# Kernel tuning notes

Hardware: AMD Instinct MI355X
Metric: run time of the kernel (lower is better)

## Reference

```python
import jax, jax.numpy as jnp
import numpy as np

NUM_LEVELS = 4
RADIUS = 4


def _avg_pool2(x):
    # x: [N, H, W] -> [N, H//2, W//2], 2x2 mean pool, stride 2 (F.avg_pool2d(corr,2,2))
    N, H, W = x.shape
    return x.reshape(N, H // 2, 2, W // 2, 2).mean(axis=(2, 4))


def _bilinear_sample(img, x, y):
    # img: [N, H, W]; x, y: [N, P] pixel coords.
    # Matches F.grid_sample(..., mode='bilinear', align_corners=True, padding_mode='zeros')
    # after the pixel->normalized->pixel round trip in bilinear_sampler (identity).
    N, H, W = img.shape
    x0 = jnp.floor(x)
    y0 = jnp.floor(y)
    wx = x - x0
    wy = y - y0
    x0i = x0.astype(jnp.int32)
    y0i = y0.astype(jnp.int32)
    flat = img.reshape(N, H * W)

    def gather(yi, xi):
        valid = (xi >= 0) & (xi <= W - 1) & (yi >= 0) & (yi <= H - 1)
        idx = jnp.clip(yi, 0, H - 1) * W + jnp.clip(xi, 0, W - 1)
        v = jnp.take_along_axis(flat, idx, axis=1)
        return jnp.where(valid, v, jnp.zeros((), img.dtype))

    v00 = gather(y0i, x0i)
    v01 = gather(y0i, x0i + 1)
    v10 = gather(y0i + 1, x0i)
    v11 = gather(y0i + 1, x0i + 1)
    return (v00 * (1 - wy) * (1 - wx) + v01 * (1 - wy) * wx
            + v10 * wy * (1 - wx) + v11 * wy * wx)


def _corr_block(fmap1, fmap2, coords):
    B, D, H, W = fmap1.shape
    # all-pairs correlation: [B, H*W, H*W] / sqrt(D)
    f1 = fmap1.reshape(B, D, H * W)
    f2 = fmap2.reshape(B, D, H * W)
    corr = jnp.einsum('bdn,bdm->bnm', f1, f2) / jnp.sqrt(jnp.asarray(D, fmap1.dtype))
    corr = corr.reshape(B * H * W, H, W)
    pyramid = [corr]
    for _ in range(NUM_LEVELS - 1):
        corr = _avg_pool2(corr)
        pyramid.append(corr)

    # coords: [B, 2, H, W] (x, y) -> [B*H*W, 2]
    c = coords.transpose(0, 2, 3, 1).reshape(B * H * W, 2)
    r = RADIUS
    d = jnp.linspace(-r, r, 2 * r + 1)
    dyg, dxg = jnp.meshgrid(d, d, indexing='ij')
    # faithful to torch: delta = stack(meshgrid(dy, dx), -1); channel 0 added to x, 1 to y
    delta = jnp.stack([dyg, dxg], axis=-1).reshape(-1, 2)  # [81, 2]

    outs = []
    for i, lvl in enumerate(pyramid):
        cl = c[:, None, :] / (2.0 ** i) + delta[None, :, :]  # [N, 81, 2]
        s = _bilinear_sample(lvl, cl[..., 0], cl[..., 1])    # [N, 81]
        outs.append(s.reshape(B, H, W, (2 * r + 1) ** 2))
    out = jnp.concatenate(outs, axis=-1)                     # [B, H, W, 4*81]
    return out.transpose(0, 3, 1, 2).astype(jnp.float32)


def setup_inputs() -> dict:
    key = jax.random.key(0)
    k1, k2, k3 = jax.random.split(key, 3)
    B, D, H, W = 2, 256, 80, 80
    fmap1 = jax.random.normal(k1, (B, D, H, W), dtype=jnp.float32)
    fmap2 = jax.random.normal(k2, (B, D, H, W), dtype=jnp.float32)
    # pixel coords in [0, W-1] x [0, H-1] (channel 0 = x, channel 1 = y)
    u = jax.random.uniform(k3, (B, 2, H, W), dtype=jnp.float32)
    scale = jnp.asarray([W - 1, H - 1], jnp.float32).reshape(1, 2, 1, 1)
    coords = u * scale
    return {"fmap1": fmap1, "fmap2": fmap2, "coords": coords}


def reference(fmap1, fmap2, coords):
    return _corr_block(fmap1, fmap2, coords)
```

## Files before the change

kernel.cpp:

```cpp
#include <hip/hip_runtime.h>


typedef _Float16 h2 __attribute__((ext_vector_type(2)));
typedef _Float16 half8 __attribute__((ext_vector_type(8)));
typedef float f32x4 __attribute__((ext_vector_type(4)));

#define HWDIM 80
#define DCH 256
#define NPIX 12800
#define NBUCKET 800
#define CHP 352

__global__ __launch_bounds__(256) void zero_k(float4* __restrict__ dst) {
    int i = blockIdx.x * 256 + threadIdx.x;
    dst[i] = make_float4(0.f, 0.f, 0.f, 0.f);
}

__global__ __launch_bounds__(256) void transpose_all(const float* __restrict__ f1,
                                                     const float* __restrict__ f2,
                                                     _Float16* __restrict__ f1h,
                                                     _Float16* __restrict__ f2p0) {
    __shared__ float tile[256][33];
    int bid = blockIdx.x;
    bool isf1 = bid < 400;
    int lb = isf1 ? bid : bid - 400;
    const float* src = isf1 ? f1 : f2;
    int b = lb / 200;
    int s0 = (lb % 200) * 32;
    int t = threadIdx.x;
    const float* sb = src + (size_t)b * DCH * (HWDIM * HWDIM);
#pragma unroll 4
    for (int k = 0; k < 32; ++k) {
        int j = t + 256 * k;
        int c = j >> 5, s = j & 31;
        tile[c][s] = sb[(size_t)c * (HWDIM * HWDIM) + s0 + s];
    }
    __syncthreads();
    int p = t & 127;
    int srow = t >> 7;
    if (isf1) {
        _Float16* db = f1h + ((size_t)b * 6400 + s0) * DCH;
#pragma unroll 4
        for (int k = 0; k < 16; ++k) {
            int s = 2 * k + srow;
            h2 v;
            v[0] = (_Float16)tile[2 * p][s];
            v[1] = (_Float16)tile[2 * p + 1][s];
            *(h2*)(db + (size_t)s * DCH + 2 * p) = v;
        }
    } else {
#pragma unroll 4
        for (int k = 0; k < 16; ++k) {
            int s = 2 * k + srow;
            int spatial = s0 + s;
            int yy = spatial / 80;
            int xx = spatial - yy * 80;
            h2 v;
            v[0] = (_Float16)tile[2 * p][s];
            v[1] = (_Float16)tile[2 * p + 1][s];
            size_t off = (size_t)b * 2073600 + (size_t)(p >> 4) * 259200
                       + ((size_t)(yy + 5) * 90 + (xx + 5)) * 32 + ((2 * p) & 31);
            *(h2*)(f2p0 + off) = v;
        }
    }
}

__global__ __launch_bounds__(256) void pools(const _Float16* __restrict__ l0,
                                             _Float16* __restrict__ l1,
                                             _Float16* __restrict__ l2,
                                             _Float16* __restrict__ l3) {
    int i = blockIdx.x * 256 + threadIdx.x;
    if (i < 409600) {
        int c2 = i & 15;
        int r = i >> 4;
        int x = r % 40; r /= 40;
        int y = r % 40; r /= 40;
        int pl = r & 7;
        int b = r >> 3;
        const h2* s = (const h2*)l0 + (size_t)b * 1036800 + (size_t)pl * 129600
                    + ((size_t)(2 * y + 5) * 90 + (2 * x + 5)) * 16 + c2;
        h2 v00 = s[0], v01 = s[16], v10 = s[90 * 16], v11 = s[90 * 16 + 16];
        float r0 = ((float)v00[0] + (float)v01[0] + (float)v10[0] + (float)v11[0]) * 0.25f;
        float r1 = ((float)v00[1] + (float)v01[1] + (float)v10[1] + (float)v11[1]) * 0.25f;
        h2 o; o[0] = (_Float16)r0; o[1] = (_Float16)r1;
        *((h2*)l1 + (size_t)b * 320000 + (size_t)pl * 40000
          + ((size_t)(y + 5) * 50 + (x + 5)) * 16 + c2) = o;
    } else if (i < 512000) {
        int j = i - 409600;
        int c2 = j & 15;
        int r = j >> 4;
        int x = r % 20; r /= 20;
        int y = r % 20; r /= 20;
        int pl = r & 7;
        int b = r >> 3;
        const h2* s = (const h2*)l0 + (size_t)b * 1036800 + (size_t)pl * 129600 + c2;
        float r0 = 0.f, r1 = 0.f;
#pragma unroll
        for (int dy = 0; dy < 4; ++dy)
#pragma unroll
            for (int dx = 0; dx < 4; ++dx) {
                h2 v = s[((size_t)(4 * y + dy + 5) * 90 + (4 * x + dx + 5)) * 16];
                r0 += (float)v[0];
                r1 += (float)v[1];
            }
        h2 o; o[0] = (_Float16)(r0 * 0.0625f); o[1] = (_Float16)(r1 * 0.0625f);
        *((h2*)l2 + (size_t)b * 115200 + (size_t)pl * 14400
          + ((size_t)(y + 5) * 30 + (x + 5)) * 16 + c2) = o;
    } else {
        int j = i - 512000;
        int c2 = j & 15;
        int r = j >> 4;
        int x = r % 10; r /= 10;
        int y = r % 10; r /= 10;
        int pl = r & 7;
        int b = r >> 3;
        const h2* s = (const h2*)l0 + (size_t)b * 1036800 + (size_t)pl * 129600 + c2;
        float r0 = 0.f, r1 = 0.f;
#pragma unroll
        for (int dy = 0; dy < 8; ++dy)
#pragma unroll
            for (int dx = 0; dx < 8; ++dx) {
                h2 v = s[((size_t)(8 * y + dy + 5) * 90 + (8 * x + dx + 5)) * 16];
                r0 += (float)v[0];
                r1 += (float)v[1];
            }
        h2 o; o[0] = (_Float16)(r0 * 0.015625f); o[1] = (_Float16)(r1 * 0.015625f);
        *((h2*)l3 + (size_t)b * 51200 + (size_t)pl * 6400
          + ((size_t)(y + 5) * 20 + (x + 5)) * 16 + c2) = o;
    }
}

static __device__ __forceinline__ int bucket_of(const float* coords, int n) {
    int b = n / 6400;
    int r = n - b * 6400;
    float cx = coords[(size_t)b * 12800 + r];
    float cy = coords[(size_t)b * 12800 + 6400 + r];
    int ix = min(max((int)floorf(cx), 0), 79);
    int iy = min(max((int)floorf(cy), 0), 79);
    return b * 400 + (iy >> 2) * 20 + (ix >> 2);
}

__global__ __launch_bounds__(1024) void bucket_k(const float* __restrict__ coords,
                                                 int* __restrict__ sortedIdxP,
                                                 int* __restrict__ rank) {
    __shared__ unsigned int histS[NBUCKET], startS[NBUCKET], curS[NBUCKET];
    __shared__ unsigned int waveSum[16];
    __shared__ unsigned int totalS;
    int t = threadIdx.x;
    if (t < NBUCKET) histS[t] = 0u;
    __syncthreads();
    int bkt[13];
#pragma unroll
    for (int i = 0; i < 13; ++i) {
        int n = i * 1024 + t;
        if (n < NPIX) {
            bkt[i] = bucket_of(coords, n);
            atomicAdd(&histS[bkt[i]], 1u);
        }
    }
    __syncthreads();
    unsigned int v = (t < NBUCKET) ? ((histS[t] + 15u) & ~15u) : 0u;
    unsigned int x = v;
#pragma unroll
    for (int d = 1; d < 64; d <<= 1) {
        unsigned int y = __shfl_up(x, d);
        if ((t & 63) >= d) x += y;
    }
    if ((t & 63) == 63) waveSum[t >> 6] = x;
    __syncthreads();
    if (t < 16) {
        unsigned int w = waveSum[t];
#pragma unroll
        for (int d = 1; d < 16; d <<= 1) {
            unsigned int y = __shfl_up(w, d);
            if (t >= d) w += y;
        }
        waveSum[t] = w;
    }
    __syncthreads();
    unsigned int incl = x + ((t >> 6) ? waveSum[(t >> 6) - 1] : 0u);
    if (t < NBUCKET) {
        unsigned int e = incl - v;
        startS[t] = e;
        curS[t] = e;
        if (t == NBUCKET - 1) totalS = incl;
    }
    __syncthreads();
#pragma unroll
    for (int i = 0; i < 13; ++i) {
        int n = i * 1024 + t;
        if (n < NPIX) {
            unsigned int pos = atomicAdd(&curS[bkt[i]], 1u);
            sortedIdxP[pos] = n;
            rank[n] = (int)pos;
        }
    }
    __syncthreads();
    if (t < NBUCKET) {
        unsigned int h = histS[t];
        if (h) {
            unsigned int pc = (h + 15u) & ~15u;
            unsigned int base = startS[t];
            int dup = sortedIdxP[base];
            for (unsigned int s = h; s < pc; ++s) sortedIdxP[base + s] = dup;
        }
    }
    for (unsigned int s = totalS + t; s < 25600u; s += 1024u) sortedIdxP[s] = -1;
}

template <int TB, int TE>
static __device__ __forceinline__ void run_tiles(
    int lane, int b,
    const _Float16* __restrict__ f2p0, const _Float16* __restrict__ f2p1,
    const _Float16* __restrict__ f2p2, const _Float16* __restrict__ f2p3,
    const int* X0cS, const int* Y0cS, const half8* bf, _Float16* G) {
#pragma unroll
    for (int tt = TB; tt < TE; ++tt) {
        const int L  = tt < 11 ? 0 : tt < 19 ? 1 : tt < 26 ? 2 : 3;
        const int rt = tt - (L == 0 ? 0 : L == 1 ? 11 : L == 2 ? 19 : 26);
        const int Ww = L == 0 ? 13 : L == 1 ? 11 : 10;
        const int MT = L == 0 ? 169 : L == 1 ? 121 : 100;
        const int MAG = L == 0 ? 161320 : L == 1 ? 190652 : 209716;
        const int Wp = L == 0 ? 90 : L == 1 ? 50 : L == 2 ? 30 : 20;
        const int PS = L == 0 ? 259200 : L == 1 ? 80000 : L == 2 ? 28800 : 12800;
        const int PB = L == 0 ? 2073600 : L == 1 ? 640000 : L == 2 ? 230400 : 102400;
        const int GO = L == 0 ? 0 : L == 1 ? 176 : L == 2 ? 304 : 416;
        const _Float16* f2L = (L == 0 ? f2p0 : L == 1 ? f2p1 : L == 2 ? f2p2 : f2p3);
        const _Float16* f2b = f2L + (size_t)b * PB
                            + ((size_t)(Y0cS[L] + 5) * Wp + (X0cS[L] + 5)) * 32;
        int m = min(rt * 16 + (lane & 15), MT - 1);
        int my = (m * MAG) >> 21;
        int mx = m - my * Ww;
        const float4* ap = (const float4*)(f2b + (size_t)(my * Wp + mx) * 32)
                         + (lane >> 4);
        half8 av[8];
#pragma unroll
        for (int kk = 0; kk < 8; ++kk)
            av[kk] = __builtin_bit_cast(half8, ap[kk * (PS / 8)]);
        __builtin_amdgcn_sched_barrier(0);
        f32x4 acc0 = {0.f, 0.f, 0.f, 0.f};
        f32x4 acc1 = {0.f, 0.f, 0.f, 0.f};
#pragma unroll
        for (int kk = 0; kk < 8; kk += 2) {
            acc0 = __builtin_amdgcn_mfma_f32_16x16x32_f16(av[kk], bf[kk], acc0, 0, 0, 0);
            acc1 = __builtin_amdgcn_mfma_f32_16x16x32_f16(av[kk + 1], bf[kk + 1], acc1, 0, 0, 0);
        }
        int gr = GO + rt * 16 + (lane >> 4) * 4;
#pragma unroll
        for (int r = 0; r < 4; ++r)
            G[(gr + r) * 17 + (lane & 15)] = (_Float16)(acc0[r] + acc1[r]);
    }
}

__global__ __launch_bounds__(512, 4) void corr_mfma(
    const _Float16* __restrict__ f1h,
    const _Float16* __restrict__ f2p0, const _Float16* __restrict__ f2p1,
    const _Float16* __restrict__ f2p2, const _Float16* __restrict__ f2p3,
    const float* __restrict__ coords, const int* __restrict__ sortedIdxP,
    _Float16* __restrict__ scratch) {
    __shared__ _Float16 G[528 * 17];
    __shared__ _Float16 f1S[16 * 264];
    __shared__ float fxS[4][16], fyS[4][16];
    __shared__ int lxS[4][16], lyS[4][16];
    __shared__ int X0cS[4], Y0cS[4], bS;

    int pphys = blockIdx.x;
    int l = (pphys & 7) * 200 + (pphys >> 3);
    int tid = threadIdx.x;
    if (sortedIdxP[l * 16] < 0) return;
    int lane = tid & 63;
    int wave = tid >> 6;

    {
        int px = tid >> 5, q = tid & 31;
        int n = sortedIdxP[l * 16 + px];
        const float4* src = (const float4*)(f1h + (size_t)n * DCH);
        *((float4*)(f1S + px * 264) + q) = src[q];
    }
    if (tid < 64) {
        int px = tid & 15, Lt = tid >> 4;
        int n = sortedIdxP[l * 16 + px];
        int b = n / 6400;
        int r = n - b * 6400;
        float cx = coords[(size_t)b * 12800 + r];
        float cy = coords[(size_t)b * 12800 + 6400 + r];
        float ls = 1.0f / (float)(1 << Lt);
        float cxl = cx * ls, cyl = cy * ls;
        float fxf = floorf(cxl), fyf = floorf(cyl);
        int X0 = (int)fxf - 4, Y0 = (int)fyf - 4;
        int ix = min(max((int)floorf(cx), 0), 79);
        int iy = min(max((int)floorf(cy), 0), 79);
        int X0c = (((ix >> 2) * 4) >> Lt) - 4;
        int Y0c = (((iy >> 2) * 4) >> Lt) - 4;
        lxS[Lt][px] = min(max(X0 - X0c, 0), 3);
        lyS[Lt][px] = min(max(Y0 - Y0c, 0), 3);
        fxS[Lt][px] = cxl - fxf;
        fyS[Lt][px] = cyl - fyf;
        X0cS[Lt] = X0c;
        Y0cS[Lt] = Y0c;
        if (tid == 0) bS = sortedIdxP[l * 16] / 6400;
    }
    __syncthreads();
    int b = bS;

    half8 bf[8];
#pragma unroll
    for (int kk = 0; kk < 8; ++kk)
        bf[kk] = *(const half8*)(f1S + (lane & 15) * 264 + ((lane >> 4) + 4 * kk) * 8);

    if      (wave == 0) run_tiles<0, 5>(lane, b, f2p0, f2p1, f2p2, f2p3, X0cS, Y0cS, bf, G);
    else if (wave == 1) run_tiles<5, 9>(lane, b, f2p0, f2p1, f2p2, f2p3, X0cS, Y0cS, bf, G);
    else if (wave == 2) run_tiles<9, 13>(lane, b, f2p0, f2p1, f2p2, f2p3, X0cS, Y0cS, bf, G);
    else if (wave == 3) run_tiles<13, 17>(lane, b, f2p0, f2p1, f2p2, f2p3, X0cS, Y0cS, bf, G);
    else if (wave == 4) run_tiles<17, 21>(lane, b, f2p0, f2p1, f2p2, f2p3, X0cS, Y0cS, bf, G);
    else if (wave == 5) run_tiles<21, 25>(lane, b, f2p0, f2p1, f2p2, f2p3, X0cS, Y0cS, bf, G);
    else if (wave == 6) run_tiles<25, 29>(lane, b, f2p0, f2p1, f2p2, f2p3, X0cS, Y0cS, bf, G);
    else                run_tiles<29, 33>(lane, b, f2p0, f2p1, f2p2, f2p3, X0cS, Y0cS, bf, G);
    __syncthreads();

    _Float16* sc = scratch + (size_t)l * 16 * CHP;
    for (int idx = tid; idx < 5184; idx += 512) {
        int k2 = idx >> 4, x = idx & 15;
        int Le = (k2 * 810) >> 16;
        int k = k2 - Le * 81;
        int Ww = Le == 0 ? 13 : Le == 1 ? 11 : 10;
        int GO = Le == 0 ? 0 : Le == 1 ? 176 : Le == 2 ? 304 : 416;
        int a = (k * 57) >> 9;
        int c = k - 9 * a;
        int gx = lxS[Le][x] + a, gy = lyS[Le][x] + c;
        int m00 = GO + gy * Ww + gx;
        float fx = fxS[Le][x], fy = fyS[Le][x];
        float t00 = (float)G[m00 * 17 + x];
        float t01 = (float)G[(m00 + 1) * 17 + x];
        float t10 = (float)G[(m00 + Ww) * 17 + x];
        float t11 = (float)G[(m00 + Ww + 1) * 17 + x];
        float v = ((1.f - fy) * ((1.f - fx) * t00 + fx * t01)
                 + fy * ((1.f - fx) * t10 + fx * t11)) * 0.0625f;
        sc[x * CHP + k2] = (_Float16)v;
    }
}

__global__ __launch_bounds__(256) void unsort_t(const _Float16* __restrict__ scratch,
                                                const int* __restrict__ rank,
                                                float* __restrict__ out) {
    __shared__ _Float16 lds[64][40];
    int blk = blockIdx.x;
    int b = blk / 100;
    int nl0 = (blk % 100) * 64;
    int t = threadIdx.x;
    int p = t >> 2, j = t & 3;
    int n = blk * 64 + p;
    int rk = rank[n];
    const float4* src = (const float4*)(scratch + (size_t)rk * CHP);
    int px = t & 63, iq = t >> 6;

    for (int c = 0; c < 11; ++c) {
        float4 f4 = src[c * 4 + j];
        *(float4*)(&lds[p][j * 8]) = f4;
        __syncthreads();
#pragma unroll
        for (int w = 0; w < 8; ++w) {
            int i = w * 4 + iq;
            int ch = c * 32 + i;
            if (ch < 324)
                out[((size_t)b * 324 + ch) * 6400 + nl0 + px] = (float)lds[px][i];
        }
        __syncthreads();
    }
}

extern "C" void kernel_launch(void* const* d_in, const int* in_sizes, int n_in,
                              void* d_out, int out_size, void* d_ws, size_t ws_size,
                              hipStream_t stream) {
    const float* fmap1 = (const float*)d_in[0];
    const float* fmap2 = (const float*)d_in[1];
    const float* coords = (const float*)d_in[2];
    float* out = (float*)d_out;
    char* ws = (char*)d_ws;

    _Float16* f1h  = (_Float16*)(ws);
    _Float16* f2p0 = (_Float16*)(ws + 6553600);
    _Float16* f2p1 = (_Float16*)(ws + 14848000);
    _Float16* f2p2 = (_Float16*)(ws + 17408000);
    _Float16* f2p3 = (_Float16*)(ws + 18329600);
    int* sortedIdxP = (int*)(ws + 18739200);
    int* rank       = (int*)(ws + 18841600);
    _Float16* scratch = (_Float16*)(ws + 18892800);

    zero_k<<<dim3(2975), dim3(256), 0, stream>>>((float4*)f2p0);

    transpose_all<<<dim3(800), dim3(256), 0, stream>>>(fmap1, fmap2, f1h, f2p0);
    pools<<<dim3(2100), dim3(256), 0, stream>>>(f2p0, f2p1, f2p2, f2p3);
    bucket_k<<<dim3(1), dim3(1024), 0, stream>>>(coords, sortedIdxP, rank);
    corr_mfma<<<dim3(1600), dim3(512), 0, stream>>>(f1h, f2p0, f2p1, f2p2, f2p3,
                                                    coords, sortedIdxP, scratch);
    unsort_t<<<dim3(200), dim3(256), 0, stream>>>(scratch, rank, out);
}
```

Measured before the change: 98.22 us.

## Software-pipeline f2 tile loads across MFMA tiles and coalesce scratch writes

After: 91.06 us. 1.08x faster.

```diff
diff --git a/kernel.cpp b/kernel.cpp
--- a/kernel.cpp
+++ b/kernel.cpp
@@ -208,51 +208,85 @@
     for (unsigned int s = totalS + t; s < 25600u; s += 1024u) sortedIdxP[s] = -1;
 }
 
+template <int TT> struct TC {
+    static constexpr int L   = TT < 11 ? 0 : TT < 19 ? 1 : TT < 26 ? 2 : 3;
+    static constexpr int rt  = TT - (L == 0 ? 0 : L == 1 ? 11 : L == 2 ? 19 : 26);
+    static constexpr int Ww  = L == 0 ? 13 : L == 1 ? 11 : 10;
+    static constexpr int MT_ = L == 0 ? 169 : L == 1 ? 121 : 100;
+    static constexpr int MAG = L == 0 ? 161320 : L == 1 ? 190652 : 209716;
+    static constexpr int Wp  = L == 0 ? 90 : L == 1 ? 50 : L == 2 ? 30 : 20;
+    static constexpr int PS  = L == 0 ? 259200 : L == 1 ? 80000 : L == 2 ? 28800 : 12800;
+    static constexpr int PB  = L == 0 ? 2073600 : L == 1 ? 640000 : L == 2 ? 230400 : 102400;
+    static constexpr int GO  = L == 0 ? 0 : L == 1 ? 176 : L == 2 ? 304 : 416;
+};
+
+template <int TT>
+static __device__ __forceinline__ void tile_load(
+    int lane, int b,
+    const _Float16* __restrict__ f2p0, const _Float16* __restrict__ f2p1,
+    const _Float16* __restrict__ f2p2, const _Float16* __restrict__ f2p3,
+    const int* X0cS, const int* Y0cS, half8 (&av)[8]) {
+    using C = TC<TT>;
+    const _Float16* f2L = (C::L == 0 ? f2p0 : C::L == 1 ? f2p1 : C::L == 2 ? f2p2 : f2p3);
+    const _Float16* f2b = f2L + (size_t)b * C::PB
+                        + ((size_t)(Y0cS[C::L] + 5) * C::Wp + (X0cS[C::L] + 5)) * 32;
+    int m = min(C::rt * 16 + (lane & 15), C::MT_ - 1);
+    int my = (m * C::MAG) >> 21;
+    int mx = m - my * C::Ww;
+    const float4* ap = (const float4*)(f2b + (size_t)(my * C::Wp + mx) * 32) + (lane >> 4);
+#pragma unroll
+    for (int kk = 0; kk < 8; ++kk)
+        av[kk] = __builtin_bit_cast(half8, ap[kk * (C::PS / 8)]);
+}
+
+template <int TT>
+static __device__ __forceinline__ void tile_mfma(
+    int lane, const half8 (&av)[8], const half8* bf, _Float16* G) {
+    using C = TC<TT>;
+    f32x4 acc0 = {0.f, 0.f, 0.f, 0.f};
+    f32x4 acc1 = {0.f, 0.f, 0.f, 0.f};
+#pragma unroll
+    for (int kk = 0; kk < 8; kk += 2) {
+        acc0 = __builtin_amdgcn_mfma_f32_16x16x32_f16(av[kk], bf[kk], acc0, 0, 0, 0);
+        acc1 = __builtin_amdgcn_mfma_f32_16x16x32_f16(av[kk + 1], bf[kk + 1], acc1, 0, 0, 0);
+    }
+    int gr = C::GO + C::rt * 16 + (lane >> 4) * 4;
+#pragma unroll
+    for (int r = 0; r < 4; ++r)
+        G[(gr + r) * 17 + (lane & 15)] = (_Float16)(acc0[r] + acc1[r]);
+}
+
+template <int TT, int TE>
+static __device__ __forceinline__ void run_pipe(
+    int lane, int b,
+    const _Float16* __restrict__ f2p0, const _Float16* __restrict__ f2p1,
+    const _Float16* __restrict__ f2p2, const _Float16* __restrict__ f2p3,
+    const int* X0cS, const int* Y0cS, const half8* bf, _Float16* G,
+    half8 (&avCur)[8]) {
+    if constexpr (TT + 1 < TE) {
+        half8 avNext[8];
+        tile_load<TT + 1>(lane, b, f2p0, f2p1, f2p2, f2p3, X0cS, Y0cS, avNext);
+        __builtin_amdgcn_sched_barrier(0);
+        tile_mfma<TT>(lane, avCur, bf, G);
+        run_pipe<TT + 1, TE>(lane, b, f2p0, f2p1, f2p2, f2p3, X0cS, Y0cS, bf, G, avNext);
+    } else {
+        __builtin_amdgcn_sched_barrier(0);
+        tile_mfma<TT>(lane, avCur, bf, G);
+    }
+}
+
 template <int TB, int TE>
 static __device__ __forceinline__ void run_tiles(
     int lane, int b,
     const _Float16* __restrict__ f2p0, const _Float16* __restrict__ f2p1,
     const _Float16* __restrict__ f2p2, const _Float16* __restrict__ f2p3,
     const int* X0cS, const int* Y0cS, const half8* bf, _Float16* G) {
-#pragma unroll
-    for (int tt = TB; tt < TE; ++tt) {
-        const int L  = tt < 11 ? 0 : tt < 19 ? 1 : tt < 26 ? 2 : 3;
-        const int rt = tt - (L == 0 ? 0 : L == 1 ? 11 : L == 2 ? 19 : 26);
-        const int Ww = L == 0 ? 13 : L == 1 ? 11 : 10;
-        const int MT = L == 0 ? 169 : L == 1 ? 121 : 100;
-        const int MAG = L == 0 ? 161320 : L == 1 ? 190652 : 209716;
-        const int Wp = L == 0 ? 90 : L == 1 ? 50 : L == 2 ? 30 : 20;
-        const int PS = L == 0 ? 259200 : L == 1 ? 80000 : L == 2 ? 28800 : 12800;
-        const int PB = L == 0 ? 2073600 : L == 1 ? 640000 : L == 2 ? 230400 : 102400;
-        const int GO = L == 0 ? 0 : L == 1 ? 176 : L == 2 ? 304 : 416;
-        const _Float16* f2L = (L == 0 ? f2p0 : L == 1 ? f2p1 : L == 2 ? f2p2 : f2p3);
-        const _Float16* f2b = f2L + (size_t)b * PB
-                            + ((size_t)(Y0cS[L] + 5) * Wp + (X0cS[L] + 5)) * 32;
-        int m = min(rt * 16 + (lane & 15), MT - 1);
-        int my = (m * MAG) >> 21;
-        int mx = m - my * Ww;
-        const float4* ap = (const float4*)(f2b + (size_t)(my * Wp + mx) * 32)
-                         + (lane >> 4);
-        half8 av[8];
-#pragma unroll
-        for (int kk = 0; kk < 8; ++kk)
-            av[kk] = __builtin_bit_cast(half8, ap[kk * (PS / 8)]);
-        __builtin_amdgcn_sched_barrier(0);
-        f32x4 acc0 = {0.f, 0.f, 0.f, 0.f};
-        f32x4 acc1 = {0.f, 0.f, 0.f, 0.f};
-#pragma unroll
-        for (int kk = 0; kk < 8; kk += 2) {
-            acc0 = __builtin_amdgcn_mfma_f32_16x16x32_f16(av[kk], bf[kk], acc0, 0, 0, 0);
-            acc1 = __builtin_amdgcn_mfma_f32_16x16x32_f16(av[kk + 1], bf[kk + 1], acc1, 0, 0, 0);
-        }
-        int gr = GO + rt * 16 + (lane >> 4) * 4;
-#pragma unroll
-        for (int r = 0; r < 4; ++r)
-            G[(gr + r) * 17 + (lane & 15)] = (_Float16)(acc0[r] + acc1[r]);
-    }
-}
-
-__global__ __launch_bounds__(512, 4) void corr_mfma(
+    half8 av0[8];
+    tile_load<TB>(lane, b, f2p0, f2p1, f2p2, f2p3, X0cS, Y0cS, av0);
+    run_pipe<TB, TE>(lane, b, f2p0, f2p1, f2p2, f2p3, X0cS, Y0cS, bf, G, av0);
+}
+
+__global__ __launch_bounds__(512, 2) void corr_mfma(
     const _Float16* __restrict__ f1h,
     const _Float16* __restrict__ f2p0, const _Float16* __restrict__ f2p1,
     const _Float16* __restrict__ f2p2, const _Float16* __restrict__ f2p3,
@@ -319,8 +353,10 @@
     __syncthreads();
 
     _Float16* sc = scratch + (size_t)l * 16 * CHP;
-    for (int idx = tid; idx < 5184; idx += 512) {
-        int k2 = idx >> 4, x = idx & 15;
+    for (int idx = tid; idx < 16 * CHP; idx += 512) {
+        int x = idx / CHP;
+        int k2 = idx - x * CHP;
+        if (k2 >= 324) continue;
         int Le = (k2 * 810) >> 16;
         int k = k2 - Le * 81;
         int Ww = Le == 0 ? 13 : Le == 1 ? 11 : 10;
@@ -336,7 +372,7 @@
         float t11 = (float)G[(m00 + Ww + 1) * 17 + x];
         float v = ((1.f - fy) * ((1.f - fx) * t00 + fx * t01)
                  + fy * ((1.f - fx) * t10 + fx * t11)) * 0.0625f;
-        sc[x * CHP + k2] = (_Float16)v;
+        sc[idx] = (_Float16)v;
     }
 }
 
```

## Split corr_mfma work per pixel group across two blocks by pyramid level

Applied to the files above, without the earlier changes.

Measured after the change: 94.61 us. 1.04x faster.

```diff
diff --git a/kernel.cpp b/kernel.cpp
--- a/kernel.cpp
+++ b/kernel.cpp
@@ -210,7 +210,7 @@
 
 template <int TB, int TE>
 static __device__ __forceinline__ void run_tiles(
-    int lane, int b,
+    int lane, int b, int goff,
     const _Float16* __restrict__ f2p0, const _Float16* __restrict__ f2p1,
     const _Float16* __restrict__ f2p2, const _Float16* __restrict__ f2p3,
     const int* X0cS, const int* Y0cS, const half8* bf, _Float16* G) {
@@ -245,7 +245,7 @@
             acc0 = __builtin_amdgcn_mfma_f32_16x16x32_f16(av[kk], bf[kk], acc0, 0, 0, 0);
             acc1 = __builtin_amdgcn_mfma_f32_16x16x32_f16(av[kk + 1], bf[kk + 1], acc1, 0, 0, 0);
         }
-        int gr = GO + rt * 16 + (lane >> 4) * 4;
+        int gr = GO - goff + rt * 16 + (lane >> 4) * 4;
 #pragma unroll
         for (int r = 0; r < 4; ++r)
             G[(gr + r) * 17 + (lane & 15)] = (_Float16)(acc0[r] + acc1[r]);
@@ -258,14 +258,16 @@
     const _Float16* __restrict__ f2p2, const _Float16* __restrict__ f2p3,
     const float* __restrict__ coords, const int* __restrict__ sortedIdxP,
     _Float16* __restrict__ scratch) {
-    __shared__ _Float16 G[528 * 17];
+    __shared__ _Float16 G[352 * 17];
     __shared__ _Float16 f1S[16 * 264];
     __shared__ float fxS[4][16], fyS[4][16];
     __shared__ int lxS[4][16], lyS[4][16];
     __shared__ int X0cS[4], Y0cS[4], bS;
 
     int pphys = blockIdx.x;
-    int l = (pphys & 7) * 200 + (pphys >> 3);
+    int lh = (pphys & 7) * 400 + (pphys >> 3);
+    int l = lh >> 1;
+    int h = lh & 1;
     int tid = threadIdx.x;
     if (sortedIdxP[l * 16] < 0) return;
     int lane = tid & 63;
@@ -308,35 +310,67 @@
     for (int kk = 0; kk < 8; ++kk)
         bf[kk] = *(const half8*)(f1S + (lane & 15) * 264 + ((lane >> 4) + 4 * kk) * 8);
 
-    if      (wave == 0) run_tiles<0, 5>(lane, b, f2p0, f2p1, f2p2, f2p3, X0cS, Y0cS, bf, G);
-    else if (wave == 1) run_tiles<5, 9>(lane, b, f2p0, f2p1, f2p2, f2p3, X0cS, Y0cS, bf, G);
-    else if (wave == 2) run_tiles<9, 13>(lane, b, f2p0, f2p1, f2p2, f2p3, X0cS, Y0cS, bf, G);
-    else if (wave == 3) run_tiles<13, 17>(lane, b, f2p0, f2p1, f2p2, f2p3, X0cS, Y0cS, bf, G);
-    else if (wave == 4) run_tiles<17, 21>(lane, b, f2p0, f2p1, f2p2, f2p3, X0cS, Y0cS, bf, G);
-    else if (wave == 5) run_tiles<21, 25>(lane, b, f2p0, f2p1, f2p2, f2p3, X0cS, Y0cS, bf, G);
-    else if (wave == 6) run_tiles<25, 29>(lane, b, f2p0, f2p1, f2p2, f2p3, X0cS, Y0cS, bf, G);
-    else                run_tiles<29, 33>(lane, b, f2p0, f2p1, f2p2, f2p3, X0cS, Y0cS, bf, G);
+    if (h == 0) {
+        if      (wave == 0) run_tiles<0, 2>(lane, b, 0, f2p0, f2p1, f2p2, f2p3, X0cS, Y0cS, bf, G);
+        else if (wave == 1) run_tiles<2, 4>(lane, b, 0, f2p0, f2p1, f2p2, f2p3, X0cS, Y0cS, bf, G);
+        else if (wave == 2) run_tiles<4, 6>(lane, b, 0, f2p0, f2p1, f2p2, f2p3, X0cS, Y0cS, bf, G);
+        else if (wave == 3) run_tiles<6, 7>(lane, b, 0, f2p0, f2p1, f2p2, f2p3, X0cS, Y0cS, bf, G);
+        else if (wave == 4) run_tiles<7, 8>(lane, b, 0, f2p0, f2p1, f2p2, f2p3, X0cS, Y0cS, bf, G);
+        else if (wave == 5) run_tiles<8, 9>(lane, b, 0, f2p0, f2p1, f2p2, f2p3, X0cS, Y0cS, bf, G);
+        else if (wave == 6) run_tiles<9, 10>(lane, b, 0, f2p0, f2p1, f2p2, f2p3, X0cS, Y0cS, bf, G);
+        else                run_tiles<10, 11>(lane, b, 0, f2p0, f2p1, f2p2, f2p3, X0cS, Y0cS, bf, G);
+    } else {
+        if      (wave == 0) run_tiles<11, 14>(lane, b, 176, f2p0, f2p1, f2p2, f2p3, X0cS, Y0cS, bf, G);
+        else if (wave == 1) run_tiles<14, 17>(lane, b, 176, f2p0, f2p1, f2p2, f2p3, X0cS, Y0cS, bf, G);
+        else if (wave == 2) run_tiles<17, 20>(lane, b, 176, f2p0, f2p1, f2p2, f2p3, X0cS, Y0cS, bf, G);
+        else if (wave == 3) run_tiles<20, 23>(lane, b, 176, f2p0, f2p1, f2p2, f2p3, X0cS, Y0cS, bf, G);
+        else if (wave == 4) run_tiles<23, 26>(lane, b, 176, f2p0, f2p1, f2p2, f2p3, X0cS, Y0cS, bf, G);
+        else if (wave == 5) run_tiles<26, 29>(lane, b, 176, f2p0, f2p1, f2p2, f2p3, X0cS, Y0cS, bf, G);
+        else if (wave == 6) run_tiles<29, 31>(lane, b, 176, f2p0, f2p1, f2p2, f2p3, X0cS, Y0cS, bf, G);
+        else                run_tiles<31, 33>(lane, b, 176, f2p0, f2p1, f2p2, f2p3, X0cS, Y0cS, bf, G);
+    }
     __syncthreads();
 
     _Float16* sc = scratch + (size_t)l * 16 * CHP;
-    for (int idx = tid; idx < 5184; idx += 512) {
-        int k2 = idx >> 4, x = idx & 15;
-        int Le = (k2 * 810) >> 16;
-        int k = k2 - Le * 81;
-        int Ww = Le == 0 ? 13 : Le == 1 ? 11 : 10;
-        int GO = Le == 0 ? 0 : Le == 1 ? 176 : Le == 2 ? 304 : 416;
-        int a = (k * 57) >> 9;
-        int c = k - 9 * a;
-        int gx = lxS[Le][x] + a, gy = lyS[Le][x] + c;
-        int m00 = GO + gy * Ww + gx;
-        float fx = fxS[Le][x], fy = fyS[Le][x];
-        float t00 = (float)G[m00 * 17 + x];
-        float t01 = (float)G[(m00 + 1) * 17 + x];
-        float t10 = (float)G[(m00 + Ww) * 17 + x];
-        float t11 = (float)G[(m00 + Ww + 1) * 17 + x];
-        float v = ((1.f - fy) * ((1.f - fx) * t00 + fx * t01)
-                 + fy * ((1.f - fx) * t10 + fx * t11)) * 0.0625f;
-        sc[x * CHP + k2] = (_Float16)v;
+    if (h == 0) {
+        for (int idx = tid; idx < 16 * 81; idx += 512) {
+            int x = (idx * 12946) >> 20;
+            int k = idx - x * 81;
+            int a = (k * 57) >> 9;
+            int c = k - 9 * a;
+            int gx = lxS[0][x] + a, gy = lyS[0][x] + c;
+            int m00 = gy * 13 + gx;
+            float fx = fxS[0][x], fy = fyS[0][x];
+            float t00 = (float)G[m00 * 17 + x];
+            float t01 = (float)G[(m00 + 1) * 17 + x];
+            float t10 = (float)G[(m00 + 13) * 17 + x];
+            float t11 = (float)G[(m00 + 14) * 17 + x];
+            float v = ((1.f - fy) * ((1.f - fx) * t00 + fx * t01)
+                     + fy * ((1.f - fx) * t10 + fx * t11)) * 0.0625f;
+            sc[x * CHP + k] = (_Float16)v;
+        }
+    } else {
+        for (int idx = tid; idx < 16 * 243; idx += 512) {
+            int x = (idx * 1079) >> 18;
+            int r = idx - x * 243;
+            int k2 = 81 + r;
+            int Le = (k2 * 810) >> 16;
+            int k = k2 - Le * 81;
+            int Ww = Le == 1 ? 11 : 10;
+            int GOr = (Le == 1 ? 176 : Le == 2 ? 304 : 416) - 176;
+            int a = (k * 57) >> 9;
+            int c = k - 9 * a;
+            int gx = lxS[Le][x] + a, gy = lyS[Le][x] + c;
+            int m00 = GOr + gy * Ww + gx;
+            float fx = fxS[Le][x], fy = fyS[Le][x];
+            float t00 = (float)G[m00 * 17 + x];
+            float t01 = (float)G[(m00 + 1) * 17 + x];
+            float t10 = (float)G[(m00 + Ww) * 17 + x];
+            float t11 = (float)G[(m00 + Ww + 1) * 17 + x];
+            float v = ((1.f - fy) * ((1.f - fx) * t00 + fx * t01)
+                     + fy * ((1.f - fx) * t10 + fx * t11)) * 0.0625f;
+            sc[x * CHP + k2] = (_Float16)v;
+        }
     }
 }
 
@@ -392,7 +426,7 @@
     transpose_all<<<dim3(800), dim3(256), 0, stream>>>(fmap1, fmap2, f1h, f2p0);
     pools<<<dim3(2100), dim3(256), 0, stream>>>(f2p0, f2p1, f2p2, f2p3);
     bucket_k<<<dim3(1), dim3(1024), 0, stream>>>(coords, sortedIdxP, rank);
-    corr_mfma<<<dim3(1600), dim3(512), 0, stream>>>(f1h, f2p0, f2p1, f2p2, f2p3,
+    corr_mfma<<<dim3(3200), dim3(512), 0, stream>>>(f1h, f2p0, f2p1, f2p2, f2p3,
                                                     coords, sortedIdxP, scratch);
     unsort_t<<<dim3(200), dim3(256), 0, stream>>>(scratch, rank, out);
 }
```

## Enlarge spatial buckets to 4x8 and process 32 pixels per block

Applied to the files above, without the earlier changes.

Result: no change. 97.16 us (-1.1%).

```diff
diff --git a/kernel.cpp b/kernel.cpp
--- a/kernel.cpp
+++ b/kernel.cpp
@@ -8,7 +8,7 @@
 #define HWDIM 80
 #define DCH 256
 #define NPIX 12800
-#define NBUCKET 800
+#define NBUCKET 400
 #define CHP 352
 
 __global__ __launch_bounds__(256) void zero_k(float4* __restrict__ dst) {
@@ -137,7 +137,7 @@
     float cy = coords[(size_t)b * 12800 + 6400 + r];
     int ix = min(max((int)floorf(cx), 0), 79);
     int iy = min(max((int)floorf(cy), 0), 79);
-    return b * 400 + (iy >> 2) * 20 + (ix >> 2);
+    return b * 200 + (iy >> 3) * 20 + (ix >> 2);
 }
 
 __global__ __launch_bounds__(1024) void bucket_k(const float* __restrict__ coords,
@@ -159,7 +159,7 @@
         }
     }
     __syncthreads();
-    unsigned int v = (t < NBUCKET) ? ((histS[t] + 15u) & ~15u) : 0u;
+    unsigned int v = (t < NBUCKET) ? ((histS[t] + 31u) & ~31u) : 0u;
     unsigned int x = v;
 #pragma unroll
     for (int d = 1; d < 64; d <<= 1) {
@@ -199,7 +199,7 @@
     if (t < NBUCKET) {
         unsigned int h = histS[t];
         if (h) {
-            unsigned int pc = (h + 15u) & ~15u;
+            unsigned int pc = (h + 31u) & ~31u;
             unsigned int base = startS[t];
             int dup = sortedIdxP[base];
             for (unsigned int s = h; s < pc; ++s) sortedIdxP[base + s] = dup;
@@ -210,21 +210,21 @@
 
 template <int TB, int TE>
 static __device__ __forceinline__ void run_tiles(
-    int lane, int b,
+    int lane, int b, int half,
     const _Float16* __restrict__ f2p0, const _Float16* __restrict__ f2p1,
     const _Float16* __restrict__ f2p2, const _Float16* __restrict__ f2p3,
     const int* X0cS, const int* Y0cS, const half8* bf, _Float16* G) {
 #pragma unroll
     for (int tt = TB; tt < TE; ++tt) {
-        const int L  = tt < 11 ? 0 : tt < 19 ? 1 : tt < 26 ? 2 : 3;
-        const int rt = tt - (L == 0 ? 0 : L == 1 ? 11 : L == 2 ? 19 : 26);
+        const int L  = tt < 14 ? 0 : tt < 23 ? 1 : tt < 30 ? 2 : 3;
+        const int rt = tt - (L == 0 ? 0 : L == 1 ? 14 : L == 2 ? 23 : 30);
         const int Ww = L == 0 ? 13 : L == 1 ? 11 : 10;
-        const int MT = L == 0 ? 169 : L == 1 ? 121 : 100;
+        const int MT = L == 0 ? 221 : L == 1 ? 143 : L == 2 ? 110 : 100;
         const int MAG = L == 0 ? 161320 : L == 1 ? 190652 : 209716;
         const int Wp = L == 0 ? 90 : L == 1 ? 50 : L == 2 ? 30 : 20;
         const int PS = L == 0 ? 259200 : L == 1 ? 80000 : L == 2 ? 28800 : 12800;
         const int PB = L == 0 ? 2073600 : L == 1 ? 640000 : L == 2 ? 230400 : 102400;
-        const int GO = L == 0 ? 0 : L == 1 ? 176 : L == 2 ? 304 : 416;
+        const int GO = L == 0 ? 0 : L == 1 ? 224 : L == 2 ? 368 : 480;
         const _Float16* f2L = (L == 0 ? f2p0 : L == 1 ? f2p1 : L == 2 ? f2p2 : f2p3);
         const _Float16* f2b = f2L + (size_t)b * PB
                             + ((size_t)(Y0cS[L] + 5) * Wp + (X0cS[L] + 5)) * 32;
@@ -248,7 +248,7 @@
         int gr = GO + rt * 16 + (lane >> 4) * 4;
 #pragma unroll
         for (int r = 0; r < 4; ++r)
-            G[(gr + r) * 17 + (lane & 15)] = (_Float16)(acc0[r] + acc1[r]);
+            G[(gr + r) * 33 + half * 16 + (lane & 15)] = (_Float16)(acc0[r] + acc1[r]);
     }
 }
 
@@ -258,28 +258,30 @@
     const _Float16* __restrict__ f2p2, const _Float16* __restrict__ f2p3,
     const float* __restrict__ coords, const int* __restrict__ sortedIdxP,
     _Float16* __restrict__ scratch) {
-    __shared__ _Float16 G[528 * 17];
-    __shared__ _Float16 f1S[16 * 264];
-    __shared__ float fxS[4][16], fyS[4][16];
-    __shared__ int lxS[4][16], lyS[4][16];
+    __shared__ _Float16 G[592 * 33];
+    __shared__ _Float16 f1S[32 * 264];
+    __shared__ float fxS[4][32], fyS[4][32];
+    __shared__ int lxS[4][32], lyS[4][32];
     __shared__ int X0cS[4], Y0cS[4], bS;
 
     int pphys = blockIdx.x;
-    int l = (pphys & 7) * 200 + (pphys >> 3);
+    int l = (pphys & 7) * 100 + (pphys >> 3);
     int tid = threadIdx.x;
-    if (sortedIdxP[l * 16] < 0) return;
+    if (sortedIdxP[l * 32] < 0) return;
     int lane = tid & 63;
     int wave = tid >> 6;
 
-    {
-        int px = tid >> 5, q = tid & 31;
-        int n = sortedIdxP[l * 16 + px];
+#pragma unroll
+    for (int uu = 0; uu < 2; ++uu) {
+        int u = tid + uu * 512;
+        int px = u >> 5, q = u & 31;
+        int n = sortedIdxP[l * 32 + px];
         const float4* src = (const float4*)(f1h + (size_t)n * DCH);
         *((float4*)(f1S + px * 264) + q) = src[q];
     }
-    if (tid < 64) {
-        int px = tid & 15, Lt = tid >> 4;
-        int n = sortedIdxP[l * 16 + px];
+    if (tid < 128) {
+        int px = tid & 31, Lt = tid >> 5;
+        int n = sortedIdxP[l * 32 + px];
         int b = n / 6400;
         int r = n - b * 6400;
         float cx = coords[(size_t)b * 12800 + r];
@@ -291,52 +293,54 @@
         int ix = min(max((int)floorf(cx), 0), 79);
         int iy = min(max((int)floorf(cy), 0), 79);
         int X0c = (((ix >> 2) * 4) >> Lt) - 4;
-        int Y0c = (((iy >> 2) * 4) >> Lt) - 4;
+        int Y0c = (((iy >> 3) * 8) >> Lt) - 4;
+        int lyMax = Lt == 0 ? 7 : Lt == 1 ? 3 : Lt == 2 ? 1 : 0;
         lxS[Lt][px] = min(max(X0 - X0c, 0), 3);
-        lyS[Lt][px] = min(max(Y0 - Y0c, 0), 3);
+        lyS[Lt][px] = min(max(Y0 - Y0c, 0), lyMax);
         fxS[Lt][px] = cxl - fxf;
         fyS[Lt][px] = cyl - fyf;
         X0cS[Lt] = X0c;
         Y0cS[Lt] = Y0c;
-        if (tid == 0) bS = sortedIdxP[l * 16] / 6400;
+        if (tid == 0) bS = sortedIdxP[l * 32] / 6400;
     }
     __syncthreads();
     int b = bS;
+    int half = wave & 1;
 
     half8 bf[8];
 #pragma unroll
     for (int kk = 0; kk < 8; ++kk)
-        bf[kk] = *(const half8*)(f1S + (lane & 15) * 264 + ((lane >> 4) + 4 * kk) * 8);
-
-    if      (wave == 0) run_tiles<0, 5>(lane, b, f2p0, f2p1, f2p2, f2p3, X0cS, Y0cS, bf, G);
-    else if (wave == 1) run_tiles<5, 9>(lane, b, f2p0, f2p1, f2p2, f2p3, X0cS, Y0cS, bf, G);
-    else if (wave == 2) run_tiles<9, 13>(lane, b, f2p0, f2p1, f2p2, f2p3, X0cS, Y0cS, bf, G);
-    else if (wave == 3) run_tiles<13, 17>(lane, b, f2p0, f2p1, f2p2, f2p3, X0cS, Y0cS, bf, G);
-    else if (wave == 4) run_tiles<17, 21>(lane, b, f2p0, f2p1, f2p2, f2p3, X0cS, Y0cS, bf, G);
-    else if (wave == 5) run_tiles<21, 25>(lane, b, f2p0, f2p1, f2p2, f2p3, X0cS, Y0cS, bf, G);
-    else if (wave == 6) run_tiles<25, 29>(lane, b, f2p0, f2p1, f2p2, f2p3, X0cS, Y0cS, bf, G);
-    else                run_tiles<29, 33>(lane, b, f2p0, f2p1, f2p2, f2p3, X0cS, Y0cS, bf, G);
-    __syncthreads();
-
-    _Float16* sc = scratch + (size_t)l * 16 * CHP;
-    for (int idx = tid; idx < 5184; idx += 512) {
-        int k2 = idx >> 4, x = idx & 15;
+        bf[kk] = *(const half8*)(f1S + (half * 16 + (lane & 15)) * 264
+                                 + ((lane >> 4) + 4 * kk) * 8);
+
+    int seg = wave >> 1;
+    if      (seg == 0) run_tiles<0, 10>(lane, b, half, f2p0, f2p1, f2p2, f2p3, X0cS, Y0cS, bf, G);
+    else if (seg == 1) run_tiles<10, 19>(lane, b, half, f2p0, f2p1, f2p2, f2p3, X0cS, Y0cS, bf, G);
+    else if (seg == 2) run_tiles<19, 28>(lane, b, half, f2p0, f2p1, f2p2, f2p3, X0cS, Y0cS, bf, G);
+    else               run_tiles<28, 37>(lane, b, half, f2p0, f2p1, f2p2, f2p3, X0cS, Y0cS, bf, G);
+    __syncthreads();
+
+    _Float16* sc = scratch + (size_t)l * 32 * CHP;
+    for (int idx = tid; idx < 32 * CHP; idx += 512) {
+        int x = (idx * 23832) >> 23;
+        int k2 = idx - x * CHP;
+        if (k2 >= 324) continue;
         int Le = (k2 * 810) >> 16;
         int k = k2 - Le * 81;
         int Ww = Le == 0 ? 13 : Le == 1 ? 11 : 10;
-        int GO = Le == 0 ? 0 : Le == 1 ? 176 : Le == 2 ? 304 : 416;
+        int GO = Le == 0 ? 0 : Le == 1 ? 224 : Le == 2 ? 368 : 480;
         int a = (k * 57) >> 9;
         int c = k - 9 * a;
         int gx = lxS[Le][x] + a, gy = lyS[Le][x] + c;
         int m00 = GO + gy * Ww + gx;
         float fx = fxS[Le][x], fy = fyS[Le][x];
-        float t00 = (float)G[m00 * 17 + x];
-        float t01 = (float)G[(m00 + 1) * 17 + x];
-        float t10 = (float)G[(m00 + Ww) * 17 + x];
-        float t11 = (float)G[(m00 + Ww + 1) * 17 + x];
+        float t00 = (float)G[m00 * 33 + x];
+        float t01 = (float)G[(m00 + 1) * 33 + x];
+        float t10 = (float)G[(m00 + Ww) * 33 + x];
+        float t11 = (float)G[(m00 + Ww + 1) * 33 + x];
         float v = ((1.f - fy) * ((1.f - fx) * t00 + fx * t01)
                  + fy * ((1.f - fx) * t10 + fx * t11)) * 0.0625f;
-        sc[x * CHP + k2] = (_Float16)v;
+        sc[idx] = (_Float16)v;
     }
 }
 
@@ -392,7 +396,7 @@
     transpose_all<<<dim3(800), dim3(256), 0, stream>>>(fmap1, fmap2, f1h, f2p0);
     pools<<<dim3(2100), dim3(256), 0, stream>>>(f2p0, f2p1, f2p2, f2p3);
     bucket_k<<<dim3(1), dim3(1024), 0, stream>>>(coords, sortedIdxP, rank);
-    corr_mfma<<<dim3(1600), dim3(512), 0, stream>>>(f1h, f2p0, f2p1, f2p2, f2p3,
-                                                    coords, sortedIdxP, scratch);
+    corr_mfma<<<dim3(800), dim3(512), 0, stream>>>(f1h, f2p0, f2p1, f2p2, f2p3,
+                                                   coords, sortedIdxP, scratch);
     unsort_t<<<dim3(200), dim3(256), 0, stream>>>(scratch, rank, out);
 }
```
